# Kernel optimization log

Measured on AMD Instinct MI355X. Metric: run time of the kernel, lower is better.

The kernel has to match this reference:

```python
import jax, jax.numpy as jnp
import numpy as np

N, C, B = 2000000, 128, 32

def setup_inputs() -> dict:
    key = jax.random.key(0)
    k1, k2 = jax.random.split(key)
    features = jax.random.normal(k1, (N, C), dtype=jnp.float32)
    batch_ids = jnp.sort(jax.random.randint(k2, (N,), 0, B, dtype=jnp.int32))
    return {"features": features, "batch_ids": batch_ids, "num_segments": B}

def reference(features, batch_ids, num_segments):
    # Global max pool per batch segment: [B, C]
    max_pool = jax.ops.segment_max(features, batch_ids, num_segments=num_segments)
    # Global avg pool per batch segment: sum / count, [B, C]
    seg_sum = jax.ops.segment_sum(features, batch_ids, num_segments=num_segments)
    counts = jax.ops.segment_sum(jnp.ones((features.shape[0],), dtype=features.dtype),
                                 batch_ids, num_segments=num_segments)
    avg_pool = seg_sum / jnp.maximum(counts, 1.0)[:, None]
    # ME.cat concatenates along the feature dimension -> [B, 2C]
    return jnp.concatenate([max_pool, avg_pool], axis=-1)
```

## Files before the change

kernel.cpp:

```cpp
#include <hip/hip_runtime.h>


using f32x4 = __attribute__((ext_vector_type(4))) float;
#define INFF __builtin_huge_valf()

#define BLOCKS 2048
#define MAXR   32

#define OFF_PART (1u << 20)

#define ACC(f) do { \
    vmax[0] = fmaxf(vmax[0], (f)[0]); \
    vmax[1] = fmaxf(vmax[1], (f)[1]); \
    vmax[2] = fmaxf(vmax[2], (f)[2]); \
    vmax[3] = fmaxf(vmax[3], (f)[3]); \
    vsum += (f); } while (0)

__global__ __launch_bounds__(256, 8)
void gp_main(const float* __restrict__ feat, const int* __restrict__ ids,
             int2* __restrict__ hdr, float* __restrict__ part, int N, int chunk) {
    const int t     = threadIdx.x;
    const int slot  = t >> 5;
    const int lane5 = t & 31;
    const int c0    = lane5 * 4;

    __shared__ int   sids[1024];
    __shared__ int   srb[MAXR + 2];
    __shared__ int   sbuf[MAXR];
    __shared__ int   snb;
    __shared__ float lmax[8][132];
    __shared__ float lsum[8][132];

    int start = blockIdx.x * chunk;
    int end   = start + chunk;
    if (end > N) end = N;
    int len = end - start;

    if (len <= 0) {
        for (int j = t; j < MAXR; j += 256)
            hdr[blockIdx.x * MAXR + j] = make_int2(0x7fffffff, 0);
        return;
    }

    for (int i = t; i < len; i += 256) sids[i] = ids[start + i];
    if (t == 0) snb = 0;
    __syncthreads();

    for (int i = t; i < len; i += 256)
        if (i > 0 && sids[i] != sids[i - 1]) {
            int p = atomicAdd(&snb, 1);
            sbuf[p] = i;
        }
    __syncthreads();
    int nb = snb;
    if (t == 0) {
        for (int a = 1; a < nb; ++a) {
            int v = sbuf[a]; int j2 = a - 1;
            while (j2 >= 0 && sbuf[j2] > v) { sbuf[j2 + 1] = sbuf[j2]; --j2; }
            sbuf[j2 + 1] = v;
        }
        srb[0] = 0;
        for (int a = 0; a < nb; ++a) srb[a + 1] = sbuf[a];
        srb[nb + 1] = len;
    }
    __syncthreads();

    const f32x4* __restrict__ frow = reinterpret_cast<const f32x4*>(feat);

    for (int j = 0; j <= nb; ++j) {
        int lrs = srb[j], lre = srb[j + 1];
        int seg = sids[lrs];
        int rs = start + lrs, re = start + lre;

        f32x4 vmax = {-INFF, -INFF, -INFF, -INFF};
        f32x4 vsum = {0.f, 0.f, 0.f, 0.f};

        int r = rs + slot;
        for (; r + 56 < re; r += 64) {
            int b0 = r * 32 + lane5;
            f32x4 f0 = __builtin_nontemporal_load(&frow[b0 +    0]);
            f32x4 f1 = __builtin_nontemporal_load(&frow[b0 +  256]);
            f32x4 f2 = __builtin_nontemporal_load(&frow[b0 +  512]);
            f32x4 f3 = __builtin_nontemporal_load(&frow[b0 +  768]);
            f32x4 f4 = __builtin_nontemporal_load(&frow[b0 + 1024]);
            f32x4 f5 = __builtin_nontemporal_load(&frow[b0 + 1280]);
            f32x4 f6 = __builtin_nontemporal_load(&frow[b0 + 1536]);
            f32x4 f7 = __builtin_nontemporal_load(&frow[b0 + 1792]);
            ACC(f0); ACC(f1); ACC(f2); ACC(f3);
            ACC(f4); ACC(f5); ACC(f6); ACC(f7);
        }
        #pragma unroll 4
        for (; r < re; r += 8) {
            f32x4 f = __builtin_nontemporal_load(&frow[r * 32 + lane5]);
            ACC(f);
        }

        lmax[slot][c0 + 0] = vmax[0]; lmax[slot][c0 + 1] = vmax[1];
        lmax[slot][c0 + 2] = vmax[2]; lmax[slot][c0 + 3] = vmax[3];
        lsum[slot][c0 + 0] = vsum[0]; lsum[slot][c0 + 1] = vsum[1];
        lsum[slot][c0 + 2] = vsum[2]; lsum[slot][c0 + 3] = vsum[3];
        __syncthreads();

        if (t < 128) {
            float m  = lmax[0][t];
            float su = lsum[0][t];
            #pragma unroll
            for (int s = 1; s < 8; ++s) {
                m   = fmaxf(m, lmax[s][t]);
                su += lsum[s][t];
            }
            size_t base = (size_t)(blockIdx.x * MAXR + j) * 256;
            part[base + t]       = m;
            part[base + 128 + t] = su;
        }
        if (t == 0) hdr[blockIdx.x * MAXR + j] = make_int2(seg, lre - lrs);
        __syncthreads();
    }
    for (int j = nb + 1 + t; j < MAXR; j += 256)
        hdr[blockIdx.x * MAXR + j] = make_int2(0x7fffffff, 0);
}

__global__ void gp_reduce(const int2* __restrict__ hdr,
                          const float* __restrict__ part,
                          float* __restrict__ out, int nblocks) {
    int b = blockIdx.x;
    int t = threadIdx.x;

    int lo = 0, hi = nblocks;
    while (lo < hi) { int mid = (lo + hi) >> 1; if (hdr[mid * MAXR].x < b) lo = mid + 1; else hi = mid; }
    int a = lo > 0 ? lo - 1 : 0;
    int lo2 = lo, hi2 = nblocks;
    while (lo2 < hi2) { int mid = (lo2 + hi2) >> 1; if (hdr[mid * MAXR].x < b + 1) lo2 = mid + 1; else hi2 = mid; }
    int c = lo2 - 1;

    float m  = -INFF;
    float su = 0.f;
    int   cnt = 0;
    for (int k = a; k <= c; ++k) {
        for (int r2 = 0; r2 < MAXR; ++r2) {
            int2 h = hdr[k * MAXR + r2];
            if (h.x == b) {
                float v = part[(size_t)(k * MAXR + r2) * 256 + t];
                m   = fmaxf(m, v);
                su += v;
                cnt += h.y;
            } else if (h.x > b) break;
        }
    }
    out[b * 256 + t] = (t < 128) ? m : su / fmaxf((float)cnt, 1.0f);
}

extern "C" void kernel_launch(void* const* d_in, const int* in_sizes, int n_in,
                              void* d_out, int out_size, void* d_ws, size_t ws_size,
                              hipStream_t stream) {
    const float* feat = (const float*)d_in[0];
    const int*   ids  = (const int*)d_in[1];
    int N = in_sizes[1];
    int C = (N > 0) ? (in_sizes[0] / N) : 128;
    int B = out_size / (2 * C);
    float* out_f = (float*)d_out;

    char*  wsb  = (char*)d_ws;
    int2*  hdr  = (int2*)wsb;
    float* part = (float*)(wsb + OFF_PART);

    int chunk = (N + BLOCKS - 1) / BLOCKS;

    gp_main<<<BLOCKS, 256, 0, stream>>>(feat, ids, hdr, part, N, chunk);
    gp_reduce<<<B, 256, 0, stream>>>(hdr, part, out_f, BLOCKS);
}
```

Measured before the change: 200.6 us.

## Fuse segment reduction into main kernel via global completion counter

Merges the partial-reduction kernel and the final per-segment reduce into one kernel. Every block bumps a global atomic counter after writing its partials. The first B blocks then spin until all blocks are done and perform the final reduction. This removes a separate kernel launch and its gap, but adds a memset of the counter and relies on all blocks being co-resident to avoid deadlock.

Measured after the change: 596.5 us. 2.97x slower.

```diff
diff --git a/kernel.cpp b/kernel.cpp
--- a/kernel.cpp
+++ b/kernel.cpp
@@ -6,7 +6,9 @@
 
 #define BLOCKS 2048
 #define MAXR   32
+#define SENT   0x7fffffff
 
+#define OFF_CNT  (896u << 10)
 #define OFF_PART (1u << 20)
 
 #define ACC(f) do { \
@@ -17,8 +19,10 @@
     vsum += (f); } while (0)
 
 __global__ __launch_bounds__(256, 8)
-void gp_main(const float* __restrict__ feat, const int* __restrict__ ids,
-             int2* __restrict__ hdr, float* __restrict__ part, int N, int chunk) {
+void gp_fused(const float* __restrict__ feat, const int* __restrict__ ids,
+              int2* __restrict__ hdr, float* __restrict__ part,
+              int* __restrict__ counter, float* __restrict__ out,
+              int N, int chunk, int nblocks, int B) {
     const int t     = threadIdx.x;
     const int slot  = t >> 5;
     const int lane5 = t & 31;
@@ -36,96 +40,102 @@
     if (end > N) end = N;
     int len = end - start;
 
-    if (len <= 0) {
+    if (len > 0) {
+        for (int i = t; i < len; i += 256) sids[i] = ids[start + i];
+        if (t == 0) snb = 0;
+        __syncthreads();
+        for (int i = t; i < len; i += 256)
+            if (i > 0 && sids[i] != sids[i - 1]) {
+                int p = atomicAdd(&snb, 1);
+                sbuf[p] = i;
+            }
+        __syncthreads();
+        int nb = snb;
+        if (t == 0) {
+            for (int a = 1; a < nb; ++a) {
+                int v = sbuf[a]; int j2 = a - 1;
+                while (j2 >= 0 && sbuf[j2] > v) { sbuf[j2 + 1] = sbuf[j2]; --j2; }
+                sbuf[j2 + 1] = v;
+            }
+            srb[0] = 0;
+            for (int a = 0; a < nb; ++a) srb[a + 1] = sbuf[a];
+            srb[nb + 1] = len;
+        }
+        __syncthreads();
+
+        const f32x4* __restrict__ frow = reinterpret_cast<const f32x4*>(feat);
+
+        for (int j = 0; j <= nb; ++j) {
+            int lrs = srb[j], lre = srb[j + 1];
+            int seg = sids[lrs];
+            int rs = start + lrs, re = start + lre;
+
+            f32x4 vmax = {-INFF, -INFF, -INFF, -INFF};
+            f32x4 vsum = {0.f, 0.f, 0.f, 0.f};
+
+            int r = rs + slot;
+            for (; r + 56 < re; r += 64) {
+                int b0 = r * 32 + lane5;
+                f32x4 f0 = __builtin_nontemporal_load(&frow[b0 +    0]);
+                f32x4 f1 = __builtin_nontemporal_load(&frow[b0 +  256]);
+                f32x4 f2 = __builtin_nontemporal_load(&frow[b0 +  512]);
+                f32x4 f3 = __builtin_nontemporal_load(&frow[b0 +  768]);
+                f32x4 f4 = __builtin_nontemporal_load(&frow[b0 + 1024]);
+                f32x4 f5 = __builtin_nontemporal_load(&frow[b0 + 1280]);
+                f32x4 f6 = __builtin_nontemporal_load(&frow[b0 + 1536]);
+                f32x4 f7 = __builtin_nontemporal_load(&frow[b0 + 1792]);
+                ACC(f0); ACC(f1); ACC(f2); ACC(f3);
+                ACC(f4); ACC(f5); ACC(f6); ACC(f7);
+            }
+            #pragma unroll 4
+            for (; r < re; r += 8) {
+                f32x4 f = __builtin_nontemporal_load(&frow[r * 32 + lane5]);
+                ACC(f);
+            }
+
+            lmax[slot][c0 + 0] = vmax[0]; lmax[slot][c0 + 1] = vmax[1];
+            lmax[slot][c0 + 2] = vmax[2]; lmax[slot][c0 + 3] = vmax[3];
+            lsum[slot][c0 + 0] = vsum[0]; lsum[slot][c0 + 1] = vsum[1];
+            lsum[slot][c0 + 2] = vsum[2]; lsum[slot][c0 + 3] = vsum[3];
+            __syncthreads();
+
+            if (t < 128) {
+                float m  = lmax[0][t];
+                float su = lsum[0][t];
+                #pragma unroll
+                for (int s = 1; s < 8; ++s) {
+                    m   = fmaxf(m, lmax[s][t]);
+                    su += lsum[s][t];
+                }
+                size_t base = (size_t)(blockIdx.x * MAXR + j) * 256;
+                part[base + t]       = m;
+                part[base + 128 + t] = su;
+            }
+            if (t == 0) hdr[blockIdx.x * MAXR + j] = make_int2(seg, lre - lrs);
+            __syncthreads();
+        }
+        for (int j = nb + 1 + t; j < MAXR; j += 256)
+            hdr[blockIdx.x * MAXR + j] = make_int2(SENT, 0);
+    } else {
         for (int j = t; j < MAXR; j += 256)
-            hdr[blockIdx.x * MAXR + j] = make_int2(0x7fffffff, 0);
-        return;
+            hdr[blockIdx.x * MAXR + j] = make_int2(SENT, 0);
     }
 
-    for (int i = t; i < len; i += 256) sids[i] = ids[start + i];
-    if (t == 0) snb = 0;
+    __threadfence();
     __syncthreads();
+    if (t == 0) atomicAdd(counter, 1);
 
-    for (int i = t; i < len; i += 256)
-        if (i > 0 && sids[i] != sids[i - 1]) {
-            int p = atomicAdd(&snb, 1);
-            sbuf[p] = i;
-        }
-    __syncthreads();
-    int nb = snb;
+    if (blockIdx.x >= B) return;
+
     if (t == 0) {
-        for (int a = 1; a < nb; ++a) {
-            int v = sbuf[a]; int j2 = a - 1;
-            while (j2 >= 0 && sbuf[j2] > v) { sbuf[j2 + 1] = sbuf[j2]; --j2; }
-            sbuf[j2 + 1] = v;
-        }
-        srb[0] = 0;
-        for (int a = 0; a < nb; ++a) srb[a + 1] = sbuf[a];
-        srb[nb + 1] = len;
+        while (__hip_atomic_load(counter, __ATOMIC_ACQUIRE,
+                                 __HIP_MEMORY_SCOPE_AGENT) < nblocks)
+            __builtin_amdgcn_s_sleep(8);
     }
     __syncthreads();
+    __threadfence();
 
-    const f32x4* __restrict__ frow = reinterpret_cast<const f32x4*>(feat);
-
-    for (int j = 0; j <= nb; ++j) {
-        int lrs = srb[j], lre = srb[j + 1];
-        int seg = sids[lrs];
-        int rs = start + lrs, re = start + lre;
-
-        f32x4 vmax = {-INFF, -INFF, -INFF, -INFF};
-        f32x4 vsum = {0.f, 0.f, 0.f, 0.f};
-
-        int r = rs + slot;
-        for (; r + 56 < re; r += 64) {
-            int b0 = r * 32 + lane5;
-            f32x4 f0 = __builtin_nontemporal_load(&frow[b0 +    0]);
-            f32x4 f1 = __builtin_nontemporal_load(&frow[b0 +  256]);
-            f32x4 f2 = __builtin_nontemporal_load(&frow[b0 +  512]);
-            f32x4 f3 = __builtin_nontemporal_load(&frow[b0 +  768]);
-            f32x4 f4 = __builtin_nontemporal_load(&frow[b0 + 1024]);
-            f32x4 f5 = __builtin_nontemporal_load(&frow[b0 + 1280]);
-            f32x4 f6 = __builtin_nontemporal_load(&frow[b0 + 1536]);
-            f32x4 f7 = __builtin_nontemporal_load(&frow[b0 + 1792]);
-            ACC(f0); ACC(f1); ACC(f2); ACC(f3);
-            ACC(f4); ACC(f5); ACC(f6); ACC(f7);
-        }
-        #pragma unroll 4
-        for (; r < re; r += 8) {
-            f32x4 f = __builtin_nontemporal_load(&frow[r * 32 + lane5]);
-            ACC(f);
-        }
-
-        lmax[slot][c0 + 0] = vmax[0]; lmax[slot][c0 + 1] = vmax[1];
-        lmax[slot][c0 + 2] = vmax[2]; lmax[slot][c0 + 3] = vmax[3];
-        lsum[slot][c0 + 0] = vsum[0]; lsum[slot][c0 + 1] = vsum[1];
-        lsum[slot][c0 + 2] = vsum[2]; lsum[slot][c0 + 3] = vsum[3];
-        __syncthreads();
-
-        if (t < 128) {
-            float m  = lmax[0][t];
-            float su = lsum[0][t];
-            #pragma unroll
-            for (int s = 1; s < 8; ++s) {
-                m   = fmaxf(m, lmax[s][t]);
-                su += lsum[s][t];
-            }
-            size_t base = (size_t)(blockIdx.x * MAXR + j) * 256;
-            part[base + t]       = m;
-            part[base + 128 + t] = su;
-        }
-        if (t == 0) hdr[blockIdx.x * MAXR + j] = make_int2(seg, lre - lrs);
-        __syncthreads();
-    }
-    for (int j = nb + 1 + t; j < MAXR; j += 256)
-        hdr[blockIdx.x * MAXR + j] = make_int2(0x7fffffff, 0);
-}
-
-__global__ void gp_reduce(const int2* __restrict__ hdr,
-                          const float* __restrict__ part,
-                          float* __restrict__ out, int nblocks) {
     int b = blockIdx.x;
-    int t = threadIdx.x;
-
     int lo = 0, hi = nblocks;
     while (lo < hi) { int mid = (lo + hi) >> 1; if (hdr[mid * MAXR].x < b) lo = mid + 1; else hi = mid; }
     int a = lo > 0 ? lo - 1 : 0;
@@ -160,12 +170,14 @@
     int B = out_size / (2 * C);
     float* out_f = (float*)d_out;
 
-    char*  wsb  = (char*)d_ws;
-    int2*  hdr  = (int2*)wsb;
-    float* part = (float*)(wsb + OFF_PART);
+    char*  wsb     = (char*)d_ws;
+    int2*  hdr     = (int2*)wsb;
+    int*   counter = (int*)(wsb + OFF_CNT);
+    float* part    = (float*)(wsb + OFF_PART);
 
     int chunk = (N + BLOCKS - 1) / BLOCKS;
 
-    gp_main<<<BLOCKS, 256, 0, stream>>>(feat, ids, hdr, part, N, chunk);
-    gp_reduce<<<B, 256, 0, stream>>>(hdr, part, out_f, BLOCKS);
+    hipMemsetAsync(counter, 0, sizeof(int), stream);
+    gp_fused<<<BLOCKS, 256, 0, stream>>>(feat, ids, hdr, part, counter, out_f,
+                                         N, chunk, BLOCKS, B);
 }
```
